# Performance work log

Hardware: AMD Instinct MI355X
Metric: run time of the kernel (lower is better)

The kernel has to match this reference:

```python
import jax, jax.numpy as jnp
import numpy as np

KP_EXTENT = 0.05
N_Q = 40000   # query points
N_S = 40000   # support points
K = 32        # neighbors per query
P = 15        # kernel points
IN_DIM = 64
OUT_DIM = 128


def setup_inputs() -> dict:
    key = jax.random.key(0)
    k1, k2, k3, k4, k5, k6 = jax.random.split(key, 6)
    q_pts = jax.random.uniform(k1, (N_Q, 3), dtype=jnp.float32)
    s_pts = jax.random.uniform(k2, (N_S, 3), dtype=jnp.float32)
    # indices in [0, N_S]; value N_S hits the appended shadow row
    neighbor_idxs = jax.random.randint(k3, (N_Q, K), 0, N_S + 1)
    x = jax.random.normal(k4, (N_S, IN_DIM), dtype=jnp.float32)
    weights = jax.random.normal(k5, (P, IN_DIM, OUT_DIM), dtype=jnp.float32) * 0.05
    kernel_points = jax.random.normal(k6, (P, 3), dtype=jnp.float32) * 0.06
    return {"q_pts": q_pts, "s_pts": s_pts, "neighbor_idxs": neighbor_idxs,
            "x": x, "weights": weights, "kernel_points": kernel_points}


def reference(q_pts, s_pts, neighbor_idxs, x, weights, kernel_points):
    # Append shadow support point. NOTE: the original does
    # zeros_like(s_pts[:1,:] + 1e6) which is exactly zeros, so shadow = origin.
    s_pad = jnp.concatenate([s_pts, jnp.zeros_like(s_pts[:1, :])], axis=0)
    # Gather neighbor coordinates, center on queries: [N, K, 3]
    neighbors = s_pad[neighbor_idxs] - q_pts[:, None, :]
    # Distances to every kernel point: [N, K, P]
    diff = neighbors[:, :, None, :] - kernel_points[None, None, :, :]
    sq_distances = jnp.sum(diff * diff, axis=3)
    all_weights = jnp.clip(1.0 - jnp.sqrt(sq_distances) / KP_EXTENT, 0.0)
    all_weights = jnp.transpose(all_weights, (0, 2, 1))  # [N, P, K]
    # Gather neighbor features with zero shadow row: [N, K, D_in]
    feats = jnp.concatenate([x, jnp.zeros_like(x[:1, :])], axis=0)
    neighbors_x = feats[neighbor_idxs]
    # Kernel-point weighted aggregation: [N, P, D_in] -> [P, N, D_in]
    weighted_features = jnp.transpose(jnp.matmul(all_weights, neighbors_x), (1, 0, 2))
    # Per-kernel-point linear map: [P, N, D_out], then sum over kernel points
    kernel_outputs = jnp.matmul(weighted_features, weights)
    output_features = jnp.sum(kernel_outputs, axis=0)  # [N, D_out]
    # Normalize by count of "valid" neighbors (feature-sum > 0 heuristic)
    neighbor_features_sum = jnp.sum(neighbors_x, axis=-1)          # [N, K]
    neighbor_num = jnp.sum(neighbor_features_sum > 0.0, axis=-1)   # [N]
    neighbor_num = jnp.maximum(neighbor_num, 1).astype(output_features.dtype)
    return output_features / neighbor_num[:, None]
```

## Files before the change

kernel.cpp:

```cpp
#include <hip/hip_runtime.h>

#define N_Q     40000
#define N_S     40000
#define KK      32
#define PP      15
#define IN_DIM  64
#define OUT_DIM 128

typedef __attribute__((ext_vector_type(8))) short short8;
typedef __attribute__((ext_vector_type(4))) float floatx4;

static __device__ __forceinline__ short f2bf(float f) {
  union { float f; unsigned u; } v; v.f = f;
  unsigned r = v.u + 0x7FFFu + ((v.u >> 16) & 1u);
  return (short)(r >> 16);
}


__global__ __launch_bounds__(256) void prep_kernel(
    const float* __restrict__ x, const float* __restrict__ s_pts,
    const float* __restrict__ weights,
    float4* __restrict__ packed, unsigned* __restrict__ wmf) {
  const int b = blockIdx.x;
  if (b < 2500) {
    const int t = b * 256 + threadIdx.x;
    const int row = t >> 4;
    const int sub = t & 15;
    float4 v = reinterpret_cast<const float4*>(x + (size_t)row * IN_DIM)[sub];
    float s = (v.x + v.y) + (v.z + v.w);
    s += __shfl_xor(s, 1, 64);
    s += __shfl_xor(s, 2, 64);
    s += __shfl_xor(s, 4, 64);
    s += __shfl_xor(s, 8, 64);
    if (sub == 0) {
      float4 pkt;
      pkt.x = s_pts[row * 3 + 0];
      pkt.y = s_pts[row * 3 + 1];
      pkt.z = s_pts[row * 3 + 2];
      pkt.w = (s > 0.0f) ? 1.0f : 0.0f;
      packed[row] = pkt;
    }
    if (t == 1) {
      float4 z; z.x = 0.f; z.y = 0.f; z.z = 0.f; z.w = 0.f;
      packed[N_S] = z;
    }
  } else {
    const int t = (b - 2500) * 256 + threadIdx.x;
    const int j2   = t & 3;
    const int lane = (t >> 2) & 63;
    const int fi   = t >> 8;
    const int kc = fi & 1, g = (fi >> 1) & 7, p = fi >> 4;
    const int c  = g * 16 + (lane & 15);
    const int k0 = kc * 32 + (lane >> 4) * 8 + 2 * j2;
    const float w0 = weights[(size_t)p * (IN_DIM * OUT_DIM) + (size_t)k0 * OUT_DIM + c];
    const float w1 = weights[(size_t)p * (IN_DIM * OUT_DIM) + (size_t)(k0 + 1) * OUT_DIM + c];
    wmf[t] = (unsigned)(unsigned short)f2bf(w0)
           | ((unsigned)(unsigned short)f2bf(w1) << 16);
  }
}

__global__ __launch_bounds__(256, 4) void kpconv_fused_kernel(
    const float* __restrict__ q_pts, const int* __restrict__ nidx,
    const float* __restrict__ x, const float* __restrict__ kpts,
    const float4* __restrict__ packed, const uint4* __restrict__ wmf4,
    float* __restrict__ out) {
  const int tid  = blockIdx.x * 256 + threadIdx.x;
  const int lane = threadIdx.x & 63;
  const int n  = tid >> 5;
  const int nA = (tid & ~63) >> 5;

  const int pl = (lane < PP) ? lane : 0;
  const float kxl = kpts[pl * 3 + 0];
  const float kyl = kpts[pl * 3 + 1];
  const float kzl = kpts[pl * 3 + 2];

  float r2 = kxl * kxl + kyl * kyl + kzl * kzl;
  #pragma unroll
  for (int s = 32; s; s >>= 1) r2 = fmaxf(r2, __shfl_xor(r2, s, 64));
  const float R  = sqrtf(r2) + 0.05f;
  const float R2 = R * R;

  const int id = nidx[tid];
  const float4 sp = packed[id];
  const bool real = (id < N_S);

  const float ox = sp.x - q_pts[n * 3 + 0];
  const float oy = sp.y - q_pts[n * 3 + 1];
  const float oz = sp.z - q_pts[n * 3 + 2];

  unsigned long long bal = __ballot(sp.w != 0.0f);
  unsigned int half = (lane < 32) ? (unsigned int)bal
                                  : (unsigned int)(bal >> 32);
  int num = (int)__popc(half);
  if (num < 1) num = 1;
  const float invnum = 1.0f / (float)num;

  floatx4 acc[8];
  #pragma unroll
  for (int g = 0; g < 8; ++g) acc[g] = (floatx4){0.f, 0.f, 0.f, 0.f};

  const float d2o = ox * ox + oy * oy + oz * oz;
  unsigned long long bc = __ballot(real && (d2o <= R2));
  while (bc) {
    const int j = (int)__ffsll((unsigned long long)bc) - 1;
    bc &= bc - 1;
    const float oxj = __shfl(ox, j);
    const float oyj = __shfl(oy, j);
    const float ozj = __shfl(oz, j);
    const int   idj = __shfl(id, j);
    const float inj = __shfl(invnum, j);
    const float dx = oxj - kxl, dy = oyj - kyl, dz = ozj - kzl;
    const float d2 = dx * dx + dy * dy + dz * dz;
    const bool hit = (lane < PP) && (d2 < 0.0025f);
    const float wc = hit ? (1.0f - 20.0f * sqrtf(d2)) * inj : 0.0f;
    unsigned long long bh = __ballot(hit);
    const int m = j >> 5;
    while (bh) {
      const int h = (int)__ffsll((unsigned long long)bh) - 1;
      bh &= bh - 1;
      const float wj = __shfl(wc, h);
      const int p = h;
      short8 af0 = {0, 0, 0, 0, 0, 0, 0, 0};
      short8 af1 = {0, 0, 0, 0, 0, 0, 0, 0};
      if ((lane & 15) == m) {
        const float4* xr = reinterpret_cast<const float4*>(x + (size_t)idj * IN_DIM);
        const int q4 = (lane >> 4) * 2;
        const float4 xa = xr[q4],     xb = xr[q4 + 1];
        const float4 xc = xr[q4 + 8], xd = xr[q4 + 9];
        af0[0] = f2bf(wj * xa.x); af0[1] = f2bf(wj * xa.y);
        af0[2] = f2bf(wj * xa.z); af0[3] = f2bf(wj * xa.w);
        af0[4] = f2bf(wj * xb.x); af0[5] = f2bf(wj * xb.y);
        af0[6] = f2bf(wj * xb.z); af0[7] = f2bf(wj * xb.w);
        af1[0] = f2bf(wj * xc.x); af1[1] = f2bf(wj * xc.y);
        af1[2] = f2bf(wj * xc.z); af1[3] = f2bf(wj * xc.w);
        af1[4] = f2bf(wj * xd.x); af1[5] = f2bf(wj * xd.y);
        af1[6] = f2bf(wj * xd.z); af1[7] = f2bf(wj * xd.w);
      }
      #pragma unroll
      for (int g = 0; g < 8; ++g) {
        const uint4 b0 = wmf4[(size_t)((p * 8 + g) * 2 + 0) * 64 + lane];
        acc[g] = __builtin_amdgcn_mfma_f32_16x16x32_bf16(
            af0, __builtin_bit_cast(short8, b0), acc[g], 0, 0, 0);
        const uint4 b1 = wmf4[(size_t)((p * 8 + g) * 2 + 1) * 64 + lane];
        acc[g] = __builtin_amdgcn_mfma_f32_16x16x32_bf16(
            af1, __builtin_bit_cast(short8, b1), acc[g], 0, 0, 0);
      }
    }
  }

  if (lane < 16) {
    #pragma unroll
    for (int g = 0; g < 8; ++g) {
      out[(size_t)nA * OUT_DIM + g * 16 + lane]       = acc[g][0];
      out[(size_t)(nA + 1) * OUT_DIM + g * 16 + lane] = acc[g][1];
    }
  }
}

extern "C" void kernel_launch(void* const* d_in, const int* in_sizes, int n_in,
                              void* d_out, int out_size, void* d_ws, size_t ws_size,
                              hipStream_t stream) {
  const float* q_pts   = (const float*)d_in[0];
  const float* s_pts   = (const float*)d_in[1];
  const int*   nidx    = (const int*)d_in[2];
  const float* x       = (const float*)d_in[3];
  const float* weights = (const float*)d_in[4];
  const float* kpts    = (const float*)d_in[5];
  float* out = (float*)d_out;

  char* ws = (char*)d_ws;
  float4*   packed = (float4*)ws;
  unsigned* wmf    = (unsigned*)(ws + (1u << 20));

  prep_kernel<<<2740, 256, 0, stream>>>(x, s_pts, weights, packed, wmf);
  kpconv_fused_kernel<<<(N_Q * KK) / 256, 256, 0, stream>>>(
      q_pts, nidx, x, kpts, packed, (const uint4*)wmf, out);
}
```

Before: 99.78 us.

## Process eight queries per wavefront to fill more MFMA rows and cut waves

Each wavefront now handles 8 query points in four passes of two queries each, instead of 2 queries per wave. All 8 queries accumulate into the same MFMA tiles, using rows 0-7 of the 16-row A operand instead of rows 0-1. The next neighbor's packed data is prefetched while the current pass runs, and candidates with no kernel-point hits are skipped before the feature gather. The change targets wave count and per-wave setup overhead, at the cost of longer serial loops per wave and fewer waves to hide latency.

```diff
diff --git a/kernel.cpp b/kernel.cpp
--- a/kernel.cpp
+++ b/kernel.cpp
@@ -64,95 +64,116 @@
     const float* __restrict__ x, const float* __restrict__ kpts,
     const float4* __restrict__ packed, const uint4* __restrict__ wmf4,
     float* __restrict__ out) {
-  const int tid  = blockIdx.x * 256 + threadIdx.x;
   const int lane = threadIdx.x & 63;
-  const int n  = tid >> 5;
-  const int nA = (tid & ~63) >> 5;
+  const int wave = threadIdx.x >> 6;
+  const int nW = (blockIdx.x * 4 + wave) * 8;
+  const size_t base = (size_t)nW * KK;
 
   const int pl = (lane < PP) ? lane : 0;
   const float kxl = kpts[pl * 3 + 0];
   const float kyl = kpts[pl * 3 + 1];
   const float kzl = kpts[pl * 3 + 2];
 
-  float r2 = kxl * kxl + kyl * kyl + kzl * kzl;
+  float r2m = kxl * kxl + kyl * kyl + kzl * kzl;
   #pragma unroll
-  for (int s = 32; s; s >>= 1) r2 = fmaxf(r2, __shfl_xor(r2, s, 64));
-  const float R  = sqrtf(r2) + 0.05f;
+  for (int s = 32; s; s >>= 1) r2m = fmaxf(r2m, __shfl_xor(r2m, s, 64));
+  const float R  = sqrtf(r2m) + 0.05f;
   const float R2 = R * R;
 
-  const int id = nidx[tid];
-  const float4 sp = packed[id];
-  const bool real = (id < N_S);
-
-  const float ox = sp.x - q_pts[n * 3 + 0];
-  const float oy = sp.y - q_pts[n * 3 + 1];
-  const float oz = sp.z - q_pts[n * 3 + 2];
-
-  unsigned long long bal = __ballot(sp.w != 0.0f);
-  unsigned int half = (lane < 32) ? (unsigned int)bal
-                                  : (unsigned int)(bal >> 32);
-  int num = (int)__popc(half);
-  if (num < 1) num = 1;
-  const float invnum = 1.0f / (float)num;
+  int ids[4];
+  #pragma unroll
+  for (int e = 0; e < 4; ++e) ids[e] = nidx[base + e * 64 + lane];
+  float qxv[4], qyv[4], qzv[4];
+  #pragma unroll
+  for (int e = 0; e < 4; ++e) {
+    const int n_e = nW + 2 * e + (lane >> 5);
+    qxv[e] = q_pts[n_e * 3 + 0];
+    qyv[e] = q_pts[n_e * 3 + 1];
+    qzv[e] = q_pts[n_e * 3 + 2];
+  }
 
   floatx4 acc[8];
   #pragma unroll
   for (int g = 0; g < 8; ++g) acc[g] = (floatx4){0.f, 0.f, 0.f, 0.f};
 
-  const float d2o = ox * ox + oy * oy + oz * oz;
-  unsigned long long bc = __ballot(real && (d2o <= R2));
-  while (bc) {
-    const int j = (int)__ffsll((unsigned long long)bc) - 1;
-    bc &= bc - 1;
-    const float oxj = __shfl(ox, j);
-    const float oyj = __shfl(oy, j);
-    const float ozj = __shfl(oz, j);
-    const int   idj = __shfl(id, j);
-    const float inj = __shfl(invnum, j);
-    const float dx = oxj - kxl, dy = oyj - kyl, dz = ozj - kzl;
-    const float d2 = dx * dx + dy * dy + dz * dz;
-    const bool hit = (lane < PP) && (d2 < 0.0025f);
-    const float wc = hit ? (1.0f - 20.0f * sqrtf(d2)) * inj : 0.0f;
-    unsigned long long bh = __ballot(hit);
-    const int m = j >> 5;
-    while (bh) {
-      const int h = (int)__ffsll((unsigned long long)bh) - 1;
-      bh &= bh - 1;
-      const float wj = __shfl(wc, h);
-      const int p = h;
-      short8 af0 = {0, 0, 0, 0, 0, 0, 0, 0};
-      short8 af1 = {0, 0, 0, 0, 0, 0, 0, 0};
-      if ((lane & 15) == m) {
-        const float4* xr = reinterpret_cast<const float4*>(x + (size_t)idj * IN_DIM);
-        const int q4 = (lane >> 4) * 2;
-        const float4 xa = xr[q4],     xb = xr[q4 + 1];
-        const float4 xc = xr[q4 + 8], xd = xr[q4 + 9];
-        af0[0] = f2bf(wj * xa.x); af0[1] = f2bf(wj * xa.y);
-        af0[2] = f2bf(wj * xa.z); af0[3] = f2bf(wj * xa.w);
-        af0[4] = f2bf(wj * xb.x); af0[5] = f2bf(wj * xb.y);
-        af0[6] = f2bf(wj * xb.z); af0[7] = f2bf(wj * xb.w);
-        af1[0] = f2bf(wj * xc.x); af1[1] = f2bf(wj * xc.y);
-        af1[2] = f2bf(wj * xc.z); af1[3] = f2bf(wj * xc.w);
-        af1[4] = f2bf(wj * xd.x); af1[5] = f2bf(wj * xd.y);
-        af1[6] = f2bf(wj * xd.z); af1[7] = f2bf(wj * xd.w);
+  float4 sp = packed[ids[0]];
+  #pragma unroll
+  for (int e = 0; e < 4; ++e) {
+    float4 spn = (float4){0.f, 0.f, 0.f, 0.f};
+    if (e < 3) spn = packed[ids[e + 1]];
+    const int id = ids[e];
+    const bool real = (id < N_S);
+
+    const float ox = sp.x - qxv[e];
+    const float oy = sp.y - qyv[e];
+    const float oz = sp.z - qzv[e];
+
+    unsigned long long bal = __ballot(sp.w != 0.0f);
+    int numA = __popc((unsigned)bal);          if (numA < 1) numA = 1;
+    int numB = __popc((unsigned)(bal >> 32));  if (numB < 1) numB = 1;
+    const float fnA = (float)numA, fnB = (float)numB;
+
+    const float d2o = ox * ox + oy * oy + oz * oz;
+    unsigned long long bc = __ballot(real && (d2o <= R2));
+    while (bc) {
+      const int j = (int)__ffsll(bc) - 1;
+      bc &= bc - 1;
+      const float oxj = __shfl(ox, j);
+      const float oyj = __shfl(oy, j);
+      const float ozj = __shfl(oz, j);
+      const float dx = oxj - kxl, dy = oyj - kyl, dz = ozj - kzl;
+      const float d2 = dx * dx + dy * dy + dz * dz;
+      const bool hit = (lane < PP) && (d2 < 0.0025f);
+      unsigned long long bh = __ballot(hit);
+      if (bh == 0ull) continue;
+
+      const float wcb = hit ? (1.0f - 20.0f * sqrtf(d2)) : 0.0f;
+      const int   idj = __shfl(id, j);
+      const float inj = 1.0f / ((j < 32) ? fnA : fnB);
+      const int   m   = 2 * e + (j >> 5);
+      while (bh) {
+        const int p = (int)__ffsll(bh) - 1;
+        bh &= bh - 1;
+        const float wj = __shfl(wcb, p) * inj;
+        short8 af0 = {0, 0, 0, 0, 0, 0, 0, 0};
+        short8 af1 = {0, 0, 0, 0, 0, 0, 0, 0};
+        if ((lane & 15) == m) {
+          const float4* xr = reinterpret_cast<const float4*>(x + (size_t)idj * IN_DIM);
+          const int q4 = (lane >> 4) * 2;
+          const float4 xa = xr[q4],     xb = xr[q4 + 1];
+          const float4 xc = xr[q4 + 8], xd = xr[q4 + 9];
+          af0[0] = f2bf(wj * xa.x); af0[1] = f2bf(wj * xa.y);
+          af0[2] = f2bf(wj * xa.z); af0[3] = f2bf(wj * xa.w);
+          af0[4] = f2bf(wj * xb.x); af0[5] = f2bf(wj * xb.y);
+          af0[6] = f2bf(wj * xb.z); af0[7] = f2bf(wj * xb.w);
+          af1[0] = f2bf(wj * xc.x); af1[1] = f2bf(wj * xc.y);
+          af1[2] = f2bf(wj * xc.z); af1[3] = f2bf(wj * xc.w);
+          af1[4] = f2bf(wj * xd.x); af1[5] = f2bf(wj * xd.y);
+          af1[6] = f2bf(wj * xd.z); af1[7] = f2bf(wj * xd.w);
+        }
+        #pragma unroll
+        for (int g = 0; g < 8; ++g) {
+          const uint4 b0 = wmf4[(size_t)((p * 8 + g) * 2 + 0) * 64 + lane];
+          acc[g] = __builtin_amdgcn_mfma_f32_16x16x32_bf16(
+              af0, __builtin_bit_cast(short8, b0), acc[g], 0, 0, 0);
+          const uint4 b1 = wmf4[(size_t)((p * 8 + g) * 2 + 1) * 64 + lane];
+          acc[g] = __builtin_amdgcn_mfma_f32_16x16x32_bf16(
+              af1, __builtin_bit_cast(short8, b1), acc[g], 0, 0, 0);
+        }
       }
+    }
+    sp = spn;
+  }
+
+  if (lane < 32) {
+    const int col = lane & 15;
+    const int rb  = (lane >> 4) * 4;
+    #pragma unroll
+    for (int r = 0; r < 4; ++r) {
       #pragma unroll
       for (int g = 0; g < 8; ++g) {
-        const uint4 b0 = wmf4[(size_t)((p * 8 + g) * 2 + 0) * 64 + lane];
-        acc[g] = __builtin_amdgcn_mfma_f32_16x16x32_bf16(
-            af0, __builtin_bit_cast(short8, b0), acc[g], 0, 0, 0);
-        const uint4 b1 = wmf4[(size_t)((p * 8 + g) * 2 + 1) * 64 + lane];
-        acc[g] = __builtin_amdgcn_mfma_f32_16x16x32_bf16(
-            af1, __builtin_bit_cast(short8, b1), acc[g], 0, 0, 0);
+        out[(size_t)(nW + rb + r) * OUT_DIM + g * 16 + col] = acc[g][r];
       }
-    }
-  }
-
-  if (lane < 16) {
-    #pragma unroll
-    for (int g = 0; g < 8; ++g) {
-      out[(size_t)nA * OUT_DIM + g * 16 + lane]       = acc[g][0];
-      out[(size_t)(nA + 1) * OUT_DIM + g * 16 + lane] = acc[g][1];
     }
   }
 }
@@ -173,6 +194,6 @@
   unsigned* wmf    = (unsigned*)(ws + (1u << 20));
 
   prep_kernel<<<2740, 256, 0, stream>>>(x, s_pts, weights, packed, wmf);
-  kpconv_fused_kernel<<<(N_Q * KK) / 256, 256, 0, stream>>>(
+  kpconv_fused_kernel<<<N_Q / 32, 256, 0, stream>>>(
       q_pts, nidx, x, kpts, packed, (const uint4*)wmf, out);
 }
```

After: 102.5 us. 1.03x slower.
